# Performance work log

Hardware: AMD Instinct MI355X
Metric: run time of the kernel (lower is better)

Reference implementation:

```python
import jax, jax.numpy as jnp
import numpy as np

D = 128
EPS = 1e-5

def group_norm1(x, gamma, beta):
    # GroupNorm with num_groups=1 over channel dim of [N, C]
    mu = jnp.mean(x, axis=-1, keepdims=True)
    var = jnp.mean(jnp.square(x - mu), axis=-1, keepdims=True)
    xhat = (x - mu) * jax.lax.rsqrt(var + EPS)
    return xhat * gamma + beta

def setup_inputs() -> dict:
    key = jax.random.key(0)
    ks = jax.random.split(key, 12)
    N_ctx, N_tgt, E = 40000, 40000, 640000
    s = 0.09  # ~1/sqrt(128) weight scale
    inp = {
        'context_feat': jax.random.normal(ks[0], (N_ctx, D), jnp.float32),
        'target_feat': jax.random.normal(ks[1], (N_tgt, D), jnp.float32),
        'context_pose': jax.random.normal(ks[2], (N_ctx, 4), jnp.float32),
        'target_pose': jax.random.normal(ks[3], (N_tgt, 4), jnp.float32),
        'W_input': s * jax.random.normal(ks[4], (D, D), jnp.float32),
        'W_rp': 0.5 * jax.random.normal(ks[5], (4, D), jnp.float32),
        'b_rp': jnp.zeros((D,), jnp.float32),
        'W_c1': s * jax.random.normal(ks[6], (2 * D, D), jnp.float32),
        'g_c1': jnp.ones((D,), jnp.float32),
        'b_c1': jnp.zeros((D,), jnp.float32),
        'W_c2': s * jax.random.normal(ks[7], (D, D), jnp.float32),
        'g_n': jnp.ones((D,), jnp.float32),
        'b_n': jnp.zeros((D,), jnp.float32),
        'W_m1': s * jax.random.normal(ks[8], (D, D), jnp.float32),
        'g_m1': jnp.ones((D,), jnp.float32),
        'bm1': jnp.zeros((D,), jnp.float32),
        'W_m2': s * jax.random.normal(ks[9], (D, D), jnp.float32),
        'g_m2': jnp.ones((D,), jnp.float32),
        'bm2': jnp.zeros((D,), jnp.float32),
        'hi': jax.random.randint(ks[10], (E,), 0, N_ctx, jnp.int32),
        'wi': jax.random.randint(ks[11], (E,), 0, N_tgt, jnp.int32),
    }
    return inp

def reference(context_feat, target_feat, context_pose, target_pose,
              W_input, W_rp, b_rp, W_c1, g_c1, b_c1, W_c2,
              g_n, b_n, W_m1, g_m1, bm1, W_m2, g_m2, bm2, hi, wi):
    # relpose: Linear(4,128) + ReLU on relative pose of each (context, target) edge
    dist_feat = context_pose[hi] - target_pose[wi]                 # [E, 4]
    dist_feat = jax.nn.relu(dist_feat @ W_rp + b_rp)               # [E, 128]
    # ctx: Linear(256,128,GN,ReLU) -> Linear(128,128, no bias)
    ctx = jnp.concatenate([context_feat[hi], dist_feat], axis=-1)  # [E, 256]
    ctx = jax.nn.relu(group_norm1(ctx @ W_c1, g_c1, b_c1))
    ctx = ctx @ W_c2                                               # [E, 128]
    # input linear + index_add scatter into targets
    tf = target_feat @ W_input                                     # [N_tgt, 128]
    tf = tf + jax.ops.segment_sum(ctx, wi, num_segments=target_feat.shape[0])
    tf = jax.nn.relu(group_norm1(tf, g_n, b_n))
    # mlp: Linear(GN,ReLU) -> Linear(GN, no act)
    tf = jax.nn.relu(group_norm1(tf @ W_m1, g_m1, bm1))
    tf = group_norm1(tf @ W_m2, g_m2, bm2)
    # residual + relu
    return jax.nn.relu(tf + target_feat)
```

## Files before the change

kernel.cpp:

```cpp
#include <hip/hip_runtime.h>

#define D 128
#define EPSV 1e-5f

typedef __attribute__((ext_vector_type(8))) __bf16 bf16x8;
typedef __attribute__((ext_vector_type(4))) float f32x4;

__device__ __forceinline__ ushort f2bf(float x) {
  unsigned u = __float_as_uint(x);
  u += 0x7fffu + ((u >> 16) & 1u);
  return (ushort)(u >> 16);
}
__device__ __forceinline__ unsigned pk2(float a, float b) {
  return (unsigned)f2bf(a) | ((unsigned)f2bf(b) << 16);
}

__global__ void k_cvt(const float* __restrict__ Wc1, const float* __restrict__ Wc2,
                      ushort* __restrict__ WT1, ushort* __restrict__ WT2) {
  int i = blockIdx.x * 256 + threadIdx.x;
  if (i < 128 * 256) {
    int n = i >> 8, k = i & 255;
    WT1[i] = f2bf(Wc1[k * 128 + n]);
  } else {
    int j = i - 128 * 256;
    if (j < 128 * 128) {
      int n = j >> 7, k = j & 127;
      WT2[j] = f2bf(Wc2[k * 128 + n]);
    }
  }
}

__global__ __launch_bounds__(256, 3) void k_edge(
    const float* __restrict__ cfeat,
    const float* __restrict__ cpose, const float* __restrict__ tpose,
    const float* __restrict__ Wrp, const float* __restrict__ brp,
    const float* __restrict__ gc1, const float* __restrict__ bc1,
    const ushort* __restrict__ WT1, const ushort* __restrict__ WT2,
    const int* __restrict__ hi, const int* __restrict__ wi,
    float* __restrict__ acc, int E) {
  __shared__ ushort Wbuf[2][4096];
  __shared__ ushort Ybuf[128 * 136];
  __shared__ float gnbuf[2][128][2];
  __shared__ int wl[128];

  const int t = threadIdx.x;
  const int lane = t & 63;
  const int wv = t >> 6;
  const int wm = wv >> 1, wn = wv & 1;
  const int s = lane & 15, g = lane >> 4;
  const int e0 = blockIdx.x * 128;

  auto stage = [&](int c, int nb) {
    const ushort* Wt = (c < 8) ? WT1 : WT2;
    const int koff = (c < 8 ? c : c - 8) * 32;
    const int krow = (c < 8) ? 256 : 128;
    const int col = t & 127, g0 = t >> 7;
#pragma unroll
    for (int v = 0; v < 2; ++v) {
      const int gg = g0 + v * 2;
      const ushort* src = Wt + (size_t)col * krow + koff + gg * 8;
      ushort* dst = &Wbuf[nb][(gg * 128 + col) * 8];
      __builtin_amdgcn_global_load_lds(
          (const __attribute__((address_space(1))) void*)src,
          (__attribute__((address_space(3))) void*)dst, 16, 0, 0);
    }
  };

  stage(0, 0);
  if (t < 128) wl[t] = wi[min(e0 + t, E - 1)];

  int hl[4];
#pragma unroll
  for (int m = 0; m < 4; ++m)
    hl[m] = hi[min(e0 + wm * 64 + m * 16 + s, E - 1)];

  {
    const int e = t >> 1;
    const int jh = (t & 1) * 64;
    const int ge = min(e0 + e, E - 1);
    const int h = hi[ge], w = wi[ge];
    float4 cp = *(const float4*)(cpose + (size_t)h * 4);
    float4 tp = *(const float4*)(tpose + (size_t)w * 4);
    const float d0 = cp.x - tp.x, d1 = cp.y - tp.y;
    const float d2 = cp.z - tp.z, d3 = cp.w - tp.w;
#pragma unroll
    for (int q = 0; q < 16; ++q) {
      const int j = jh + q * 4;
      float4 b  = *(const float4*)(brp + j);
      float4 w0 = *(const float4*)(Wrp + j);
      float4 w1 = *(const float4*)(Wrp + D + j);
      float4 w2 = *(const float4*)(Wrp + 2 * D + j);
      float4 w3 = *(const float4*)(Wrp + 3 * D + j);
      float r0 = fmaxf(b.x + d0 * w0.x + d1 * w1.x + d2 * w2.x + d3 * w3.x, 0.f);
      float r1 = fmaxf(b.y + d0 * w0.y + d1 * w1.y + d2 * w2.y + d3 * w3.y, 0.f);
      float r2 = fmaxf(b.z + d0 * w0.z + d1 * w1.z + d2 * w2.z + d3 * w3.z, 0.f);
      float r3 = fmaxf(b.w + d0 * w0.w + d1 * w1.w + d2 * w2.w + d3 * w3.w, 0.f);
      *(uint2*)&Ybuf[e * 136 + j] = make_uint2(pk2(r0, r1), pk2(r2, r3));
    }
  }
  __syncthreads();

  f32x4 acc1[4][4];
#pragma unroll
  for (int m = 0; m < 4; ++m)
#pragma unroll
    for (int n = 0; n < 4; ++n) acc1[m][n] = (f32x4){0.f, 0.f, 0.f, 0.f};

  for (int kc = 0; kc < 8; ++kc) {
    const int nb = kc & 1;
    stage(kc + 1, nb ^ 1);
    bf16x8 a[4];
    if (kc < 4) {
#pragma unroll
      for (int m = 0; m < 4; ++m) {
        const float* src = cfeat + (size_t)hl[m] * D + kc * 32 + g * 8;
        float4 f0 = *(const float4*)src;
        float4 f1 = *(const float4*)(src + 4);
        union { uint4 u; bf16x8 v; } cv;
        cv.u.x = pk2(f0.x, f0.y); cv.u.y = pk2(f0.z, f0.w);
        cv.u.z = pk2(f1.x, f1.y); cv.u.w = pk2(f1.z, f1.w);
        a[m] = cv.v;
      }
    } else {
#pragma unroll
      for (int m = 0; m < 4; ++m)
        a[m] = *(const bf16x8*)
            &Ybuf[(wm * 64 + m * 16 + s) * 136 + (kc - 4) * 32 + g * 8];
    }
#pragma unroll
    for (int n = 0; n < 4; ++n) {
      bf16x8 b = *(const bf16x8*)
          &Wbuf[nb][(g * 128 + wn * 64 + n * 16 + s) * 8];
#pragma unroll
      for (int m = 0; m < 4; ++m)
        acc1[m][n] =
            __builtin_amdgcn_mfma_f32_16x16x32_bf16(a[m], b, acc1[m][n], 0, 0, 0);
    }
    __syncthreads();
  }

#pragma unroll
  for (int m = 0; m < 4; ++m) {
#pragma unroll
    for (int reg = 0; reg < 4; ++reg) {
      float p1 = acc1[m][0][reg] + acc1[m][1][reg] + acc1[m][2][reg] +
                 acc1[m][3][reg];
      float p2 = acc1[m][0][reg] * acc1[m][0][reg] +
                 acc1[m][1][reg] * acc1[m][1][reg] +
                 acc1[m][2][reg] * acc1[m][2][reg] +
                 acc1[m][3][reg] * acc1[m][3][reg];
#pragma unroll
      for (int msk = 1; msk < 16; msk <<= 1) {
        p1 += __shfl_xor(p1, msk, 64);
        p2 += __shfl_xor(p2, msk, 64);
      }
      if (s == 0) {
        const int row = wm * 64 + m * 16 + g * 4 + reg;
        *(float2*)&gnbuf[wn][row][0] = make_float2(p1, p2);
      }
    }
  }
  __syncthreads();
  {
    float gcl[4], bcl[4];
#pragma unroll
    for (int n = 0; n < 4; ++n) {
      gcl[n] = gc1[wn * 64 + n * 16 + s];
      bcl[n] = bc1[wn * 64 + n * 16 + s];
    }
#pragma unroll
    for (int m = 0; m < 4; ++m) {
#pragma unroll
      for (int reg = 0; reg < 4; ++reg) {
        const int row = wm * 64 + m * 16 + g * 4 + reg;
        float2 q0 = *(const float2*)&gnbuf[0][row][0];
        float2 q1 = *(const float2*)&gnbuf[1][row][0];
        const float mean = (q0.x + q1.x) * (1.f / 128.f);
        const float var = (q0.y + q1.y) * (1.f / 128.f) - mean * mean;
        const float rstd = rsqrtf(var + EPSV);
#pragma unroll
        for (int n = 0; n < 4; ++n) {
          float y = (acc1[m][n][reg] - mean) * rstd * gcl[n] + bcl[n];
          Ybuf[row * 136 + wn * 64 + n * 16 + s] = f2bf(fmaxf(y, 0.f));
        }
      }
    }
  }
  __syncthreads();

  f32x4 acc2[4][4];
#pragma unroll
  for (int m = 0; m < 4; ++m)
#pragma unroll
    for (int n = 0; n < 4; ++n) acc2[m][n] = (f32x4){0.f, 0.f, 0.f, 0.f};

  for (int kc = 0; kc < 4; ++kc) {
    const int c = 8 + kc;
    const int nb = c & 1;
    if (c < 11) stage(c + 1, nb ^ 1);
    bf16x8 a[4];
#pragma unroll
    for (int m = 0; m < 4; ++m)
      a[m] = *(const bf16x8*)
          &Ybuf[(wm * 64 + m * 16 + s) * 136 + kc * 32 + g * 8];
#pragma unroll
    for (int n = 0; n < 4; ++n) {
      bf16x8 b = *(const bf16x8*)
          &Wbuf[nb][(g * 128 + wn * 64 + n * 16 + s) * 8];
#pragma unroll
      for (int m = 0; m < 4; ++m)
        acc2[m][n] =
            __builtin_amdgcn_mfma_f32_16x16x32_bf16(a[m], b, acc2[m][n], 0, 0, 0);
    }
    if (kc < 3) __syncthreads();
  }

#pragma unroll
  for (int m = 0; m < 4; ++m) {
#pragma unroll
    for (int reg = 0; reg < 4; ++reg) {
      const int rl = wm * 64 + m * 16 + g * 4 + reg;
      if (e0 + rl < E) {
        const int w = wl[rl];
        float* base = acc + (size_t)w * D + wn * 64 + s;
#pragma unroll
        for (int n = 0; n < 4; ++n)
          unsafeAtomicAdd(base + n * 16, acc2[m][n][reg]);
      }
    }
  }
}

__device__ __forceinline__ void reduce16(float& a, float& b) {
#pragma unroll
  for (int w = 1; w < 16; w <<= 1) {
    a += __shfl_xor(a, w, 64);
    b += __shfl_xor(b, w, 64);
  }
}

__global__ __launch_bounds__(256, 2) void k_input(
    const float* __restrict__ tfeat, const float* __restrict__ Wi,
    float* __restrict__ acc, int N) {
  __shared__ float Wbuf[64][132];
  __shared__ float xt[64][132];
  const int t = threadIdx.x;
  const int r = t >> 4, s = t & 15, j0 = s * 8;
  const int row0 = blockIdx.x * 64;

  for (int idx = t; idx < 64 * 32; idx += 256) {
    int rr = idx >> 5, c4 = idx & 31;
    int grow = row0 + rr;
    float4 v = make_float4(0.f, 0.f, 0.f, 0.f);
    if (grow < N) v = *(const float4*)(tfeat + (size_t)grow * D + c4 * 4);
    *(float4*)&xt[rr][c4 * 4] = v;
  }

  float a[4][8] = {};
  for (int kc = 0; kc < 2; ++kc) {
    __syncthreads();
    for (int idx = t; idx < 64 * 32; idx += 256) {
      int kk = idx >> 5, c4 = idx & 31;
      *(float4*)&Wbuf[kk][c4 * 4] =
          *(const float4*)(Wi + (size_t)(kc * 64 + kk) * D + c4 * 4);
    }
    __syncthreads();
#pragma unroll 4
    for (int kk = 0; kk < 64; ++kk) {
      float4 w0 = *(const float4*)&Wbuf[kk][j0];
      float4 w1 = *(const float4*)&Wbuf[kk][j0 + 4];
#pragma unroll
      for (int i = 0; i < 4; ++i) {
        float xv = xt[r + 16 * i][kc * 64 + kk];
        a[i][0] += xv * w0.x; a[i][1] += xv * w0.y;
        a[i][2] += xv * w0.z; a[i][3] += xv * w0.w;
        a[i][4] += xv * w1.x; a[i][5] += xv * w1.y;
        a[i][6] += xv * w1.z; a[i][7] += xv * w1.w;
      }
    }
  }
#pragma unroll
  for (int i = 0; i < 4; ++i) {
    int row = row0 + r + 16 * i;
    if (row < N) {
      *(float4*)(acc + (size_t)row * D + j0) =
          make_float4(a[i][0], a[i][1], a[i][2], a[i][3]);
      *(float4*)(acc + (size_t)row * D + j0 + 4) =
          make_float4(a[i][4], a[i][5], a[i][6], a[i][7]);
    }
  }
}

__global__ __launch_bounds__(256, 2) void k_node(
    const float* __restrict__ tfeat,
    const float* __restrict__ gn, const float* __restrict__ bn,
    const float* __restrict__ Wm1, const float* __restrict__ gm1,
    const float* __restrict__ bm1,
    const float* __restrict__ Wm2, const float* __restrict__ gm2,
    const float* __restrict__ bm2,
    float* __restrict__ acc, int N) {
  __shared__ float Wbuf[64][132];
  __shared__ float xt[64][132];
  const int t = threadIdx.x;
  const int r = t >> 4, s = t & 15, j0 = s * 8;
  const int row0 = blockIdx.x * 64;

  auto stageW = [&](const float* W, int kc) {
    for (int idx = t; idx < 64 * 32; idx += 256) {
      int kk = idx >> 5, c4 = idx & 31;
      *(float4*)&Wbuf[kk][c4 * 4] =
          *(const float4*)(W + (size_t)(kc * 64 + kk) * D + c4 * 4);
    }
  };
  auto gemm = [&](float a[4][8], int kc) {
#pragma unroll 4
    for (int kk = 0; kk < 64; ++kk) {
      float4 w0 = *(const float4*)&Wbuf[kk][j0];
      float4 w1 = *(const float4*)&Wbuf[kk][j0 + 4];
#pragma unroll
      for (int i = 0; i < 4; ++i) {
        float xv = xt[r + 16 * i][kc * 64 + kk];
        a[i][0] += xv * w0.x; a[i][1] += xv * w0.y;
        a[i][2] += xv * w0.z; a[i][3] += xv * w0.w;
        a[i][4] += xv * w1.x; a[i][5] += xv * w1.y;
        a[i][6] += xv * w1.z; a[i][7] += xv * w1.w;
      }
    }
  };

  {
    float gv[8], bv[8];
#pragma unroll
    for (int m = 0; m < 8; ++m) { gv[m] = gn[j0 + m]; bv[m] = bn[j0 + m]; }
#pragma unroll
    for (int i = 0; i < 4; ++i) {
      int row = row0 + r + 16 * i;
      float v[8] = {};
      if (row < N) {
        float4 v0 = *(const float4*)(acc + (size_t)row * D + j0);
        float4 v1 = *(const float4*)(acc + (size_t)row * D + j0 + 4);
        v[0] = v0.x; v[1] = v0.y; v[2] = v0.z; v[3] = v0.w;
        v[4] = v1.x; v[5] = v1.y; v[6] = v1.z; v[7] = v1.w;
      }
      float s1 = 0.f, s2 = 0.f;
#pragma unroll
      for (int m = 0; m < 8; ++m) { s1 += v[m]; s2 += v[m] * v[m]; }
      reduce16(s1, s2);
      float mean = s1 * (1.f / 128.f);
      float var = s2 * (1.f / 128.f) - mean * mean;
      float rstd = rsqrtf(var + EPSV);
#pragma unroll
      for (int m = 0; m < 8; ++m)
        xt[r + 16 * i][j0 + m] = fmaxf((v[m] - mean) * rstd * gv[m] + bv[m], 0.f);
    }
  }

  float a[4][8] = {};
  for (int kc = 0; kc < 2; ++kc) {
    __syncthreads();
    stageW(Wm1, kc);
    __syncthreads();
    gemm(a, kc);
  }
  __syncthreads();
  {
    float gv[8], bv[8];
#pragma unroll
    for (int m = 0; m < 8; ++m) { gv[m] = gm1[j0 + m]; bv[m] = bm1[j0 + m]; }
#pragma unroll
    for (int i = 0; i < 4; ++i) {
      float s1 = 0.f, s2 = 0.f;
#pragma unroll
      for (int m = 0; m < 8; ++m) { s1 += a[i][m]; s2 += a[i][m] * a[i][m]; }
      reduce16(s1, s2);
      float mean = s1 * (1.f / 128.f);
      float var = s2 * (1.f / 128.f) - mean * mean;
      float rstd = rsqrtf(var + EPSV);
#pragma unroll
      for (int m = 0; m < 8; ++m)
        xt[r + 16 * i][j0 + m] =
            fmaxf((a[i][m] - mean) * rstd * gv[m] + bv[m], 0.f);
    }
  }

  float a2[4][8] = {};
  for (int kc = 0; kc < 2; ++kc) {
    __syncthreads();
    stageW(Wm2, kc);
    __syncthreads();
    gemm(a2, kc);
  }
  {
    float gv[8], bv[8];
#pragma unroll
    for (int m = 0; m < 8; ++m) { gv[m] = gm2[j0 + m]; bv[m] = bm2[j0 + m]; }
#pragma unroll
    for (int i = 0; i < 4; ++i) {
      int row = row0 + r + 16 * i;
      float s1 = 0.f, s2 = 0.f;
#pragma unroll
      for (int m = 0; m < 8; ++m) { s1 += a2[i][m]; s2 += a2[i][m] * a2[i][m]; }
      reduce16(s1, s2);
      float mean = s1 * (1.f / 128.f);
      float var = s2 * (1.f / 128.f) - mean * mean;
      float rstd = rsqrtf(var + EPSV);
      if (row < N) {
        float o[8];
#pragma unroll
        for (int m = 0; m < 8; ++m) {
          float x = (a2[i][m] - mean) * rstd * gv[m] + bv[m];
          o[m] = fmaxf(x + tfeat[(size_t)row * D + j0 + m], 0.f);
        }
        *(float4*)(acc + (size_t)row * D + j0) =
            make_float4(o[0], o[1], o[2], o[3]);
        *(float4*)(acc + (size_t)row * D + j0 + 4) =
            make_float4(o[4], o[5], o[6], o[7]);
      }
    }
  }
}

extern "C" void kernel_launch(void* const* d_in, const int* in_sizes, int n_in,
                              void* d_out, int out_size, void* d_ws,
                              size_t ws_size, hipStream_t stream) {
  const float* cfeat = (const float*)d_in[0];
  const float* tfeat = (const float*)d_in[1];
  const float* cpose = (const float*)d_in[2];
  const float* tpose = (const float*)d_in[3];
  const float* Wi    = (const float*)d_in[4];
  const float* Wrp   = (const float*)d_in[5];
  const float* brp   = (const float*)d_in[6];
  const float* Wc1   = (const float*)d_in[7];
  const float* gc1   = (const float*)d_in[8];
  const float* bc1   = (const float*)d_in[9];
  const float* Wc2   = (const float*)d_in[10];
  const float* gn    = (const float*)d_in[11];
  const float* bn    = (const float*)d_in[12];
  const float* Wm1   = (const float*)d_in[13];
  const float* gm1   = (const float*)d_in[14];
  const float* bm1   = (const float*)d_in[15];
  const float* Wm2   = (const float*)d_in[16];
  const float* gm2   = (const float*)d_in[17];
  const float* bm2   = (const float*)d_in[18];
  const int* hi      = (const int*)d_in[19];
  const int* wi      = (const int*)d_in[20];

  const int N = in_sizes[1] / D;
  const int E = in_sizes[19];
  float* out = (float*)d_out;

  ushort* WT1 = (ushort*)d_ws;
  ushort* WT2 = WT1 + 128 * 256;

  const int nbN = (N + 63) / 64;
  const int nbE = (E + 127) / 128;

  k_cvt<<<192, 256, 0, stream>>>(Wc1, Wc2, WT1, WT2);
  k_input<<<nbN, 256, 0, stream>>>(tfeat, Wi, out, N);
  k_edge<<<nbE, 256, 0, stream>>>(cfeat, cpose, tpose, Wrp, brp, gc1, bc1,
                                  WT1, WT2, hi, wi, out, E);
  k_node<<<nbN, 256, 0, stream>>>(tfeat, gn, bn, Wm1, gm1, bm1, Wm2, gm2, bm2,
                                  out, N);
}
```

Baseline: 457.5 us.

## Sort edges by target via counting sort and pre-reduce runs before atomics

Adds a counting-sort pipeline (histogram, three-pass scan, ordering) that permutes edges by target index. The edge kernel processes edges in this order, stages the per-edge outputs in LDS as bf16, and sums consecutive rows that share a target before issuing one atomic per run and column. The aim is to cut global atomic traffic and contention in the scatter-add. The cost is five extra kernel launches, random gathers of hi/wi through the permutation, and an extra bf16 rounding of edge outputs before summation.

After: 512.6 us. 1.12x slower.

```diff
diff --git a/kernel.cpp b/kernel.cpp
--- a/kernel.cpp
+++ b/kernel.cpp
@@ -13,6 +13,9 @@
 }
 __device__ __forceinline__ unsigned pk2(float a, float b) {
   return (unsigned)f2bf(a) | ((unsigned)f2bf(b) << 16);
+}
+__device__ __forceinline__ float bf2f(ushort u) {
+  return __uint_as_float((unsigned)u << 16);
 }
 
 __global__ void k_cvt(const float* __restrict__ Wc1, const float* __restrict__ Wc2,
@@ -30,6 +33,63 @@
   }
 }
 
+__global__ void k_hist(const int* __restrict__ wi, int* __restrict__ hist, int E) {
+  int i = blockIdx.x * 256 + threadIdx.x;
+  if (i < E) atomicAdd(&hist[wi[i]], 1);
+}
+
+__global__ void k_scan1(const int* __restrict__ hist, int* __restrict__ bsum, int Nt) {
+  __shared__ int sd[256];
+  int t = threadIdx.x, i = blockIdx.x * 256 + t;
+  sd[t] = (i < Nt) ? hist[i] : 0;
+  __syncthreads();
+  for (int off = 128; off > 0; off >>= 1) {
+    if (t < off) sd[t] += sd[t + off];
+    __syncthreads();
+  }
+  if (t == 0) bsum[blockIdx.x] = sd[0];
+}
+
+__global__ void k_scan2(const int* __restrict__ bsum, int* __restrict__ bpre, int nc) {
+  __shared__ int sd[256];
+  int t = threadIdx.x;
+  int v = (t < nc) ? bsum[t] : 0;
+  sd[t] = v;
+  __syncthreads();
+  for (int off = 1; off < 256; off <<= 1) {
+    int x = (t >= off) ? sd[t - off] : 0;
+    __syncthreads();
+    sd[t] += x;
+    __syncthreads();
+  }
+  if (t < nc) bpre[t] = sd[t] - v;
+}
+
+__global__ void k_scan3(const int* __restrict__ hist, const int* __restrict__ bpre,
+                        int* __restrict__ cursor, int Nt) {
+  __shared__ int sd[256];
+  int t = threadIdx.x, i = blockIdx.x * 256 + t;
+  int v = (i < Nt) ? hist[i] : 0;
+  sd[t] = v;
+  __syncthreads();
+  for (int off = 1; off < 256; off <<= 1) {
+    int x = (t >= off) ? sd[t - off] : 0;
+    __syncthreads();
+    sd[t] += x;
+    __syncthreads();
+  }
+  if (i < Nt) cursor[i] = bpre[blockIdx.x] + sd[t] - v;
+}
+
+__global__ void k_order(const int* __restrict__ wi, int* __restrict__ cursor,
+                        int* __restrict__ order, int E) {
+  int i = blockIdx.x * 256 + threadIdx.x;
+  if (i < E) {
+    int p = atomicAdd(&cursor[wi[i]], 1);
+    order[p] = i;
+  }
+}
+
 __global__ __launch_bounds__(256, 3) void k_edge(
     const float* __restrict__ cfeat,
     const float* __restrict__ cpose, const float* __restrict__ tpose,
@@ -37,11 +97,15 @@
     const float* __restrict__ gc1, const float* __restrict__ bc1,
     const ushort* __restrict__ WT1, const ushort* __restrict__ WT2,
     const int* __restrict__ hi, const int* __restrict__ wi,
+    const int* __restrict__ order,
     float* __restrict__ acc, int E) {
   __shared__ ushort Wbuf[2][4096];
   __shared__ ushort Ybuf[128 * 136];
   __shared__ float gnbuf[2][128][2];
   __shared__ int wl[128];
+  __shared__ int runstart[129];
+  __shared__ int nruns_s;
+  __shared__ unsigned long long mask0_s;
 
   const int t = threadIdx.x;
   const int lane = t & 63;
@@ -49,6 +113,11 @@
   const int wm = wv >> 1, wn = wv & 1;
   const int s = lane & 15, g = lane >> 4;
   const int e0 = blockIdx.x * 128;
+
+  auto eidOf = [&](int p) {
+    p = min(p, E - 1);
+    return order ? order[p] : p;
+  };
 
   auto stage = [&](int c, int nb) {
     const ushort* Wt = (c < 8) ? WT1 : WT2;
@@ -67,17 +136,17 @@
   };
 
   stage(0, 0);
-  if (t < 128) wl[t] = wi[min(e0 + t, E - 1)];
+  if (t < 128) wl[t] = wi[eidOf(e0 + t)];
 
   int hl[4];
 #pragma unroll
   for (int m = 0; m < 4; ++m)
-    hl[m] = hi[min(e0 + wm * 64 + m * 16 + s, E - 1)];
+    hl[m] = hi[eidOf(e0 + wm * 64 + m * 16 + s)];
 
   {
     const int e = t >> 1;
     const int jh = (t & 1) * 64;
-    const int ge = min(e0 + e, E - 1);
+    const int ge = eidOf(e0 + e);
     const int h = hi[ge], w = wi[ge];
     float4 cp = *(const float4*)(cpose + (size_t)h * 4);
     float4 tp = *(const float4*)(tpose + (size_t)w * 4);
@@ -161,6 +230,7 @@
     }
   }
   __syncthreads();
+
   {
     float gcl[4], bcl[4];
 #pragma unroll
@@ -215,18 +285,47 @@
     if (kc < 3) __syncthreads();
   }
 
+  bool head = false;
+  if (t < 128) head = (t == 0) || (wl[t] != wl[t - 1]);
+  unsigned long long bm = __ballot(head);
+  if (t == 0) mask0_s = bm;
+  __syncthreads();
+
+  if (t < 128) {
+    const int base = (t >= 64) ? __popcll(mask0_s) : 0;
+    const int rank = base + __popcll(bm & ((1ULL << lane) - 1));
+    if (head) runstart[rank] = t;
+    if (t == 64) nruns_s = __popcll(mask0_s) + __popcll(bm);
+  }
+  if (t == 127 && false) {}
+
 #pragma unroll
   for (int m = 0; m < 4; ++m) {
 #pragma unroll
     for (int reg = 0; reg < 4; ++reg) {
-      const int rl = wm * 64 + m * 16 + g * 4 + reg;
-      if (e0 + rl < E) {
-        const int w = wl[rl];
-        float* base = acc + (size_t)w * D + wn * 64 + s;
-#pragma unroll
-        for (int n = 0; n < 4; ++n)
-          unsafeAtomicAdd(base + n * 16, acc2[m][n][reg]);
-      }
+      const int row = wm * 64 + m * 16 + g * 4 + reg;
+      const bool vld = (e0 + row) < E;
+      const int sw = (row & 7) << 3;
+#pragma unroll
+      for (int n = 0; n < 4; ++n) {
+        const int col = wn * 64 + n * 16 + s;
+        Ybuf[row * 128 + (col ^ sw)] = vld ? f2bf(acc2[m][n][reg]) : (ushort)0;
+      }
+    }
+  }
+  __syncthreads();
+
+  {
+    const int nr = nruns_s;
+    for (int task = t; task < (nr << 7); task += 256) {
+      const int run = task >> 7, col = task & 127;
+      const int r0 = runstart[run];
+      const int r1 = (run + 1 < nr) ? runstart[run + 1] : 128;
+      const int w = wl[r0];
+      float sum = 0.f;
+      for (int r = r0; r < r1; ++r)
+        sum += bf2f(Ybuf[r * 128 + (col ^ ((r & 7) << 3))]);
+      unsafeAtomicAdd(acc + (size_t)w * D + col, sum);
     }
   }
 }
@@ -312,7 +411,7 @@
           *(const float4*)(W + (size_t)(kc * 64 + kk) * D + c4 * 4);
     }
   };
-  auto gemm = [&](float a[4][8], int kc) {
+  auto gemm = [&](float (&a)[4][8], int kc) {
 #pragma unroll 4
     for (int kk = 0; kk < 64; ++kk) {
       float4 w0 = *(const float4*)&Wbuf[kk][j0];
@@ -449,16 +548,37 @@
   const int E = in_sizes[19];
   float* out = (float*)d_out;
 
-  ushort* WT1 = (ushort*)d_ws;
-  ushort* WT2 = WT1 + 128 * 256;
+  uint8_t* ws = (uint8_t*)d_ws;
+  ushort* WT1 = (ushort*)ws;
+  ushort* WT2 = (ushort*)(ws + 65536);
+  size_t off = 98304;
+  int* hist   = (int*)(ws + off); off += (size_t)N * 4;
+  int* cursor = (int*)(ws + off); off += (size_t)N * 4;
+  int* bsum   = (int*)(ws + off); off += 1024;
+  int* bpre   = (int*)(ws + off); off += 1024;
+  int* order  = (int*)(ws + off); off += (size_t)E * 4;
+
+  const int nchunks = (N + 255) / 256;
+  const bool sorted = (ws_size >= off) && (nchunks <= 256);
 
   const int nbN = (N + 63) / 64;
   const int nbE = (E + 127) / 128;
+  const int nbEthr = (E + 255) / 256;
+
+  if (sorted) {
+    hipMemsetAsync(hist, 0, (size_t)N * 4, stream);
+    k_hist<<<nbEthr, 256, 0, stream>>>(wi, hist, E);
+    k_scan1<<<nchunks, 256, 0, stream>>>(hist, bsum, N);
+    k_scan2<<<1, 256, 0, stream>>>(bsum, bpre, nchunks);
+    k_scan3<<<nchunks, 256, 0, stream>>>(hist, bpre, cursor, N);
+    k_order<<<nbEthr, 256, 0, stream>>>(wi, cursor, order, E);
+  }
 
   k_cvt<<<192, 256, 0, stream>>>(Wc1, Wc2, WT1, WT2);
   k_input<<<nbN, 256, 0, stream>>>(tfeat, Wi, out, N);
   k_edge<<<nbE, 256, 0, stream>>>(cfeat, cpose, tpose, Wrp, brp, gc1, bc1,
-                                  WT1, WT2, hi, wi, out, E);
+                                  WT1, WT2, hi, wi, sorted ? order : nullptr,
+                                  out, E);
   k_node<<<nbN, 256, 0, stream>>>(tfeat, gn, bn, Wm1, gm1, bm1, Wm2, gm2, bm2,
                                   out, N);
 }
```
